# Kernel optimization log

Measured on AMD Instinct MI355X. Metric: run time of the kernel, lower is better.

## Reference

```python
import jax, jax.numpy as jnp
import numpy as np

B, T, S, D, H = 2, 2048, 2048, 2048, 16
HD = D // H  # 128
SCALE = 1.0 / np.sqrt(HD)


def _rope(x, cos, sin):
    # x: [B,H,S,HD]; cos/sin: [1,1,S,HD//2]
    b, h, s, d = x.shape
    xs = x.reshape(b, h, s, d // 2, 2)
    x0, x1 = xs[..., 0], xs[..., 1]
    rot = jnp.stack([x0 * cos - x1 * sin, x1 * cos + x0 * sin], axis=-1)
    return rot.reshape(b, h, s, d)


def _split_heads(x):
    b, s, _ = x.shape
    return x.reshape(b, s, H, HD).transpose(0, 2, 1, 3)


def setup_inputs() -> dict:
    key = jax.random.key(0)
    ks = jax.random.split(key, 6)
    w_std = (1.0 / np.sqrt(2.0)) * np.sqrt(6.0 / (D + D))  # xavier_uniform with gain 1/sqrt(2)
    def xavier(k):
        return jax.random.uniform(k, (D, D), jnp.float32, -w_std, w_std)
    # rotary tables (standard inv-freq form)
    inv_freq = 1.0 / (10000.0 ** (np.arange(0, HD, 2, dtype=np.float32) / HD))  # [HD//2]
    ang = np.arange(T, dtype=np.float32)[:, None] * inv_freq[None, :]           # [T,HD//2]
    cos = jnp.asarray(np.cos(ang), jnp.float32)[None, None]  # [1,1,T,HD//2]
    sin = jnp.asarray(np.sin(ang), jnp.float32)[None, None]
    return {
        "hidden_states": jax.random.normal(ks[0], (B, T, D), jnp.float32),
        "encoder_hidden_states": jax.random.normal(ks[1], (B, S, D), jnp.float32),
        "Wq": xavier(ks[2]),
        "Wk": xavier(ks[3]),
        "Wv": xavier(ks[4]),
        "Wo": xavier(ks[5]),
        "cos_q": cos, "sin_q": sin,
        "cos_k": cos, "sin_k": sin,
    }


def reference(hidden_states, encoder_hidden_states, Wq, Wk, Wv, Wo,
              cos_q, sin_q, cos_k, sin_k):
    # Linear (no bias): y = x @ W.T
    q = _split_heads(jnp.einsum('btd,ed->bte', hidden_states, Wq))          # [B,H,T,HD]
    k = _split_heads(jnp.einsum('bsd,ed->bse', encoder_hidden_states, Wk))  # [B,H,S,HD]
    v = _split_heads(jnp.einsum('bsd,ed->bse', encoder_hidden_states, Wv))  # [B,H,S,HD]
    q = _rope(q, cos_q, sin_q)
    k = _rope(k, cos_k, sin_k)
    scores = jnp.einsum('bhtd,bhsd->bhts', q, k) * SCALE                    # [B,H,T,S]
    attn = jax.nn.softmax(scores.astype(jnp.float32), axis=-1)
    ctx = jnp.einsum('bhts,bhsd->bhtd', attn, v)                            # [B,H,T,HD]
    ctx = ctx.transpose(0, 2, 1, 3).reshape(B, T, D)                        # merge heads
    return jnp.einsum('btd,ed->bte', ctx, Wo)
```

## Files before the change

kernel.cpp:

```cpp
#include <hip/hip_runtime.h>
#include <cmath>

#define SCALE_F 0.088388347648318447f

typedef _Float16 f16;
typedef _Float16 f16x8 __attribute__((ext_vector_type(8)));
typedef _Float16 f16x4 __attribute__((ext_vector_type(4)));
typedef float f32x4 __attribute__((ext_vector_type(4)));
typedef float f32x16 __attribute__((ext_vector_type(16)));
typedef unsigned int u32;
typedef unsigned int u32x4 __attribute__((ext_vector_type(4)));

#define MFMA16(a, b, c) __builtin_amdgcn_mfma_f32_16x16x32_f16(a, b, c, 0, 0, 0)
#define MFMA32(a, b, c) __builtin_amdgcn_mfma_f32_32x32x16_f16(a, b, c, 0, 0, 0)
#define Z16 ((f32x16){0.f,0.f,0.f,0.f,0.f,0.f,0.f,0.f,0.f,0.f,0.f,0.f,0.f,0.f,0.f,0.f})
#define EX2(x) __builtin_amdgcn_exp2f(x)

__device__ __forceinline__ void gl2lds16(const f16* g, f16* l) {
    __builtin_amdgcn_global_load_lds(
        (const __attribute__((address_space(1))) unsigned int*)g,
        (__attribute__((address_space(3))) unsigned int*)l, 16, 0, 0);
}

__device__ __forceinline__ u32 pk2(float x, float y) {
    const unsigned short a = __builtin_bit_cast(unsigned short, (f16)x);
    const unsigned short b = __builtin_bit_cast(unsigned short, (f16)y);
    return (u32)a | ((u32)b << 16);
}
__device__ __forceinline__ float fswapsum(float x) {
    u32 a = __builtin_bit_cast(u32, x), b;
    asm volatile("v_mov_b32 %0, %1" : "=&v"(b) : "v"(a));
    asm volatile("v_permlane32_swap_b32 %0, %1" : "+v"(a), "+v"(b));
    return __builtin_bit_cast(float, a) + __builtin_bit_cast(float, b);
}
__device__ __forceinline__ float fswapmax(float x) {
    u32 a = __builtin_bit_cast(u32, x), b;
    asm volatile("v_mov_b32 %0, %1" : "=&v"(b) : "v"(a));
    asm volatile("v_permlane32_swap_b32 %0, %1" : "+v"(a), "+v"(b));
    return fmaxf(__builtin_bit_cast(float, a), __builtin_bit_cast(float, b));
}

__global__ __launch_bounds__(256) void cvt_all(
    const float* __restrict__ hs, const float* __restrict__ es,
    const float* __restrict__ Wq, const float* __restrict__ Wk,
    const float* __restrict__ Wv, const float* __restrict__ Wo,
    f16* __restrict__ dst)
{
    const int c = blockIdx.x * 256 + threadIdx.x;
    const float* src; int off;
    if (c < 2097152) { src = (c < 1048576) ? hs : es; off = c & 1048575; }
    else {
        const int cc = c - 2097152;
        const int wsel = cc >> 19; off = cc & 524287;
        src = wsel == 0 ? Wq : wsel == 1 ? Wk : wsel == 2 ? Wv : Wo;
    }
    const float4* p = (const float4*)src + (size_t)off * 2;
    const float4 a = p[0], b2 = p[1];
    f16x8 o = {(f16)a.x, (f16)a.y, (f16)a.z, (f16)a.w,
               (f16)b2.x, (f16)b2.y, (f16)b2.z, (f16)b2.w};
    *(f16x8*)(dst + (size_t)c * 8) = o;
}

template <int OUT_MODE>
__global__ __launch_bounds__(256, 2) void gemm16(
    const f16* __restrict__ A, const f16* __restrict__ W,
    void* __restrict__ Cv, int M, int N, int K,
    const float* __restrict__ Cs, const float* __restrict__ Sn)
{
    __shared__ __align__(16) f16 Al[128 * 64];
    __shared__ __align__(16) f16 Bl[128 * 64];
    const int tid = threadIdx.x;
    const int l = tid & 63, w = tid >> 6;
    const int wr = w >> 1, wc = w & 1;

    const int nwg = gridDim.x, cpx = nwg >> 3;
    const int bid = blockIdx.x;
    const int swz = (bid & 7) * cpx + (bid >> 3);
    const int nbn = N >> 7;
    const int bm = (swz / nbn) * 128, bn = (swz % nbn) * 128;

    f32x4 acc[4][4];
#pragma unroll
    for (int i = 0; i < 4; ++i)
#pragma unroll
        for (int j = 0; j < 4; ++j) acc[i][j] = (f32x4){0.f, 0.f, 0.f, 0.f};

    const int srow = tid >> 3;
    const int sg = tid & 7;

    for (int k0 = 0; k0 < K; k0 += 64) {
        __syncthreads();
#pragma unroll
        for (int i = 0; i < 4; ++i) {
            const int row = i * 32 + srow;
            const int lg = sg ^ (row & 7);
            gl2lds16(A + (size_t)(bm + row) * K + k0 + lg * 8, Al + row * 64 + sg * 8);
            gl2lds16(W + (size_t)(bn + row) * K + k0 + lg * 8, Bl + row * 64 + sg * 8);
        }
        __syncthreads();
#pragma unroll
        for (int kk = 0; kk < 2; ++kk) {
            f16x8 a[4], b[4];
            const int g = kk * 4 + (l >> 4);
#pragma unroll
            for (int m = 0; m < 4; ++m) {
                const int row = wr * 64 + m * 16 + (l & 15);
                a[m] = *(const f16x8*)(Al + row * 64 + (g ^ (row & 7)) * 8);
            }
#pragma unroll
            for (int n = 0; n < 4; ++n) {
                const int row = wc * 64 + n * 16 + (l & 15);
                b[n] = *(const f16x8*)(Bl + row * 64 + (g ^ (row & 7)) * 8);
            }
#pragma unroll
            for (int m = 0; m < 4; ++m)
#pragma unroll
                for (int n = 0; n < 4; ++n)
                    acc[m][n] = MFMA16(a[m], b[n], acc[m][n]);
        }
    }

#pragma unroll
    for (int m = 0; m < 4; ++m)
#pragma unroll
        for (int n = 0; n < 4; ++n)
#pragma unroll
            for (int j = 0; j < 4; ++j) {
                const int r = bm + wr * 64 + m * 16 + ((l >> 4) << 2) + j;
                const int c = bn + wc * 64 + n * 16 + (l & 15);
                if (OUT_MODE == 0) {
                    ((f16*)Cv)[(size_t)r * N + c] = (f16)acc[m][n][j];
                } else if (OUT_MODE == 2) {
                    ((float*)Cv)[(size_t)r * N + c] = acc[m][n][j];
                } else if (OUT_MODE == 3) {
                    ((f16*)Cv)[(size_t)((c >> 11) * 2048 + r) * 2048 + (c & 2047)] = (f16)acc[m][n][j];
                } else if (OUT_MODE == 4) {
                    const float v = acc[m][n][j];
                    const float vp = __shfl_xor(v, 1);
                    const int t = r & 2047;
                    const int i2 = (c & 127) >> 1;
                    const float co = Cs[t * 64 + i2];
                    const float si = Sn[t * 64 + i2];
                    const float y = (c & 1) ? fmaf(v, co, vp * si) : fmaf(v, co, -vp * si);
                    ((f16*)Cv)[(size_t)r * N + c] = (f16)y;
                }
            }
}

__global__ __launch_bounds__(256, 2) void attn16(
    const f16* __restrict__ Qg, const f16* __restrict__ Kg,
    const f16* __restrict__ Vt, f16* __restrict__ Og)
{
    __shared__ __align__(16) f16 Kl[2][64 * 128];
    __shared__ __align__(16) f16 Vl[2][128 * 64];
    __shared__ float bnc[4][32];

    const int tid = threadIdx.x;
    const int l = tid & 63, w = tid >> 6;
    const int l31 = l & 31, hi = l >> 5;
    const int hi4 = hi * 4;

    const int bid = blockIdx.x;
    const int swz = (bid & 7) * 64 + (bid >> 3);
    const int bh = swz >> 4, qt = swz & 15;
    const int b = bh >> 4, h = bh & 15;

    const int qrow = b * 2048 + qt * 128 + w * 32 + l31;
    const f16 qsc = (f16)(0.088388347648318447f * 1.44269504088896f);
    f16x8 qf[8];
#pragma unroll
    for (int kc = 0; kc < 8; ++kc) {
        f16x8 t0 = *(const f16x8*)(Qg + (size_t)qrow * 2048 + h * 128 + kc * 16 + hi * 8);
#pragma unroll
        for (int e = 0; e < 8; ++e) t0[e] = t0[e] * qsc;
        qf[kc] = t0;
    }

    f32x16 o[4] = {Z16, Z16, Z16, Z16};
    float mrow = -3.0e38f, lrow = 0.0f;

    const f16* Kbase = Kg + (size_t)(b * 2048) * 2048 + h * 128;
    const f16* Vbase = Vt + (size_t)(b * 2048 + h * 128) * 2048;

#define STAGE(buf, st) do {                                                              \
    _Pragma("unroll")                                                                    \
    for (int u = 0; u < 4; ++u) {                                                        \
        const int idx = u * 256 + tid; const int row = idx >> 4, g = idx & 15;           \
        gl2lds16(Kbase + (size_t)((st) + row) * 2048 + (g ^ (row & 15)) * 8,             \
                 &Kl[buf][row * 128 + g * 8]);                                           \
    }                                                                                    \
    _Pragma("unroll")                                                                    \
    for (int u = 0; u < 4; ++u) {                                                        \
        const int idx = u * 256 + tid; const int d = idx >> 3, g = idx & 7;              \
        gl2lds16(Vbase + (size_t)d * 2048 + (st) + (g ^ (d & 7)) * 8,                    \
                 &Vl[buf][d * 64 + g * 8]);                                              \
    }                                                                                    \
} while (0)

    STAGE(0, 0);
    __syncthreads();

    int cur = 0;
    for (int t = 0; t < 32; ++t) {
        if (t < 31) STAGE(cur ^ 1, (t + 1) * 64);
        const f16* Kc = Kl[cur];
        const f16* Vc = Vl[cur];

        f32x16 p0 = Z16, p1 = Z16;
        __builtin_amdgcn_s_setprio(1);
#pragma unroll
        for (int kc = 0; kc < 8; ++kc) {
            const int g = ((kc * 2 + hi) ^ (l31 & 15)) * 8;
            const f16x8 k0 = *(const f16x8*)(Kc + l31 * 128 + g);
            const f16x8 k1 = *(const f16x8*)(Kc + (32 + l31) * 128 + g);
            p0 = MFMA32(k0, qf[kc], p0);
            p1 = MFMA32(k1, qf[kc], p1);
        }
        __builtin_amdgcn_s_setprio(0);

        float mt[16];
#pragma unroll
        for (int r = 0; r < 16; ++r) mt[r] = fmaxf(p0[r], p1[r]);
#pragma unroll
        for (int r = 0; r < 8; ++r) mt[r] = fmaxf(mt[r], mt[r + 8]);
#pragma unroll
        for (int r = 0; r < 4; ++r) mt[r] = fmaxf(mt[r], mt[r + 4]);
        float mx = fmaxf(fmaxf(mt[0], mt[1]), fmaxf(mt[2], mt[3]));
        mx = fswapmax(mx);

        if (!__all(mx <= mrow + 8.0f)) {
            const float mn = fmaxf(mrow, mx);
            const float cr = EX2(mrow - mn);
            mrow = mn;
            lrow *= cr;
            if (hi == 0) bnc[w][l31] = cr;
#pragma unroll
            for (int r = 0; r < 16; ++r) {
                const float crr = bnc[w][(r & 3) + 8 * (r >> 2) + 4 * hi];
                o[0][r] *= crr; o[1][r] *= crr; o[2][r] *= crr; o[3][r] *= crr;
            }
        }

        float st16[16];
#pragma unroll
        for (int r = 0; r < 16; ++r) {
            p0[r] = EX2(p0[r] - mrow);
            p1[r] = EX2(p1[r] - mrow);
            st16[r] = p0[r] + p1[r];
        }
#pragma unroll
        for (int r = 0; r < 8; ++r) st16[r] += st16[r + 8];
#pragma unroll
        for (int r = 0; r < 4; ++r) st16[r] += st16[r + 4];
        lrow += fswapsum((st16[0] + st16[1]) + (st16[2] + st16[3]));

        f16x8 pf[4];
#pragma unroll
        for (int ksl = 0; ksl < 2; ++ksl) {
            u32x4 w0 = {pk2(p0[8*ksl+0], p0[8*ksl+1]), pk2(p0[8*ksl+2], p0[8*ksl+3]),
                        pk2(p0[8*ksl+4], p0[8*ksl+5]), pk2(p0[8*ksl+6], p0[8*ksl+7])};
            pf[ksl] = __builtin_bit_cast(f16x8, w0);
            u32x4 w1 = {pk2(p1[8*ksl+0], p1[8*ksl+1]), pk2(p1[8*ksl+2], p1[8*ksl+3]),
                        pk2(p1[8*ksl+4], p1[8*ksl+5]), pk2(p1[8*ksl+6], p1[8*ksl+7])};
            pf[2 + ksl] = __builtin_bit_cast(f16x8, w1);
        }

        __builtin_amdgcn_s_setprio(1);
#pragma unroll
        for (int dt = 0; dt < 4; ++dt) {
            const f16* vrow = Vc + (dt * 32 + l31) * 64;
#pragma unroll
            for (int ks = 0; ks < 4; ++ks) {
                const f16x4 vlo = *(const f16x4*)(vrow + ((ks * 2)     ^ (l31 & 7)) * 8 + hi4);
                const f16x4 vhi = *(const f16x4*)(vrow + ((ks * 2 + 1) ^ (l31 & 7)) * 8 + hi4);
                const f16x8 vf = __builtin_shufflevector(vlo, vhi, 0, 1, 2, 3, 4, 5, 6, 7);
                o[dt] = MFMA32(pf[ks], vf, o[dt]);
            }
        }
        __builtin_amdgcn_s_setprio(0);

        __syncthreads();
        cur ^= 1;
    }
#undef STAGE

    const float inv = 1.0f / lrow;
    if (hi == 0) bnc[w][l31] = inv;
#pragma unroll
    for (int r = 0; r < 16; ++r) {
        const int qq = (r & 3) + 8 * (r >> 2) + 4 * hi;
        const float ir = bnc[w][qq];
        const size_t row = (size_t)(b * 2048 + qt * 128 + w * 32 + qq);
#pragma unroll
        for (int dt = 0; dt < 4; ++dt)
            Og[row * 2048 + h * 128 + dt * 32 + l31] = (f16)(o[dt][r] * ir);
    }
}

extern "C" void kernel_launch(void* const* d_in, const int* in_sizes, int n_in,
                              void* d_out, int out_size, void* d_ws, size_t ws_size,
                              hipStream_t stream) {
    const float* hs = (const float*)d_in[0];
    const float* es = (const float*)d_in[1];
    const float* Wq = (const float*)d_in[2];
    const float* Wk = (const float*)d_in[3];
    const float* Wv = (const float*)d_in[4];
    const float* Wo = (const float*)d_in[5];
    const float* cq = (const float*)d_in[6];
    const float* sq = (const float*)d_in[7];
    const float* ck = (const float*)d_in[8];
    const float* sk = (const float*)d_in[9];
    float* out = (float*)d_out;

    f16* hs16 = (f16*)d_ws;
    f16* es16 = hs16 + 8388608;
    f16* Wq16 = es16 + 8388608;
    f16* Wk16 = Wq16 + 4194304;
    f16* Wv16 = Wk16 + 4194304;
    f16* Wo16 = Wv16 + 4194304;
    f16* Q16  = Wo16 + 4194304;
    f16* K16  = Q16 + 8388608;
    f16* Vt16 = K16 + 8388608;
    f16* ctx16 = hs16;

    const dim3 tB(256);
    cvt_all<<<dim3(16384), tB, 0, stream>>>(hs, es, Wq, Wk, Wv, Wo, hs16);

    gemm16<4><<<dim3(512), tB, 0, stream>>>(hs16, Wq16, Q16, 4096, 2048, 2048, cq, sq);
    gemm16<4><<<dim3(512), tB, 0, stream>>>(es16, Wk16, K16, 4096, 2048, 2048, ck, sk);
    gemm16<3><<<dim3(512), tB, 0, stream>>>(Wv16, es16, Vt16, 2048, 4096, 2048, nullptr, nullptr);

    attn16<<<dim3(512), tB, 0, stream>>>(Q16, K16, Vt16, ctx16);

    gemm16<2><<<dim3(512), tB, 0, stream>>>(ctx16, Wo16, out, 4096, 2048, 2048, nullptr, nullptr);
}
```

Measured before the change: 292.6 us.

## Stage K/V through registers into padded LDS instead of direct global-to-LDS loads

New measurement: 290.1 us. Within noise of the previous version (-0.8%).

```diff
diff --git a/kernel.cpp b/kernel.cpp
--- a/kernel.cpp
+++ b/kernel.cpp
@@ -9,6 +9,7 @@
 typedef float f32x4 __attribute__((ext_vector_type(4)));
 typedef float f32x16 __attribute__((ext_vector_type(16)));
 typedef unsigned int u32;
+typedef unsigned int u32x2 __attribute__((ext_vector_type(2)));
 typedef unsigned int u32x4 __attribute__((ext_vector_type(4)));
 
 #define MFMA16(a, b, c) __builtin_amdgcn_mfma_f32_16x16x32_f16(a, b, c, 0, 0, 0)
@@ -151,8 +152,8 @@
     const f16* __restrict__ Qg, const f16* __restrict__ Kg,
     const f16* __restrict__ Vt, f16* __restrict__ Og)
 {
-    __shared__ __align__(16) f16 Kl[2][64 * 128];
-    __shared__ __align__(16) f16 Vl[2][128 * 64];
+    __shared__ __align__(16) f16 Kl[2][64 * 132];
+    __shared__ __align__(16) f16 Vl[2][128 * 68];
     __shared__ float bnc[4][32];
 
     const int tid = threadIdx.x;
@@ -160,6 +161,9 @@
     const int l31 = l & 31, hi = l >> 5;
     const int hi4 = hi * 4;
 
+    const int krow = tid >> 4, kg = tid & 15;
+    const int vd = tid >> 3, vg = tid & 7;
+
     const int bid = blockIdx.x;
     const int swz = (bid & 7) * 64 + (bid >> 3);
     const int bh = swz >> 4, qt = swz & 15;
@@ -182,27 +186,39 @@
     const f16* Kbase = Kg + (size_t)(b * 2048) * 2048 + h * 128;
     const f16* Vbase = Vt + (size_t)(b * 2048 + h * 128) * 2048;
 
-#define STAGE(buf, st) do {                                                              \
+    u32x4 kst[4], vst[4];
+
+#define LOADT(st) do {                                                                   \
+    _Pragma("unroll")                                                                    \
+    for (int u = 0; u < 4; ++u)                                                          \
+        kst[u] = *(const u32x4*)(Kbase + (size_t)((st) + krow + u * 16) * 2048 + kg * 8);\
+    _Pragma("unroll")                                                                    \
+    for (int u = 0; u < 4; ++u)                                                          \
+        vst[u] = *(const u32x4*)(Vbase + (size_t)(vd + u * 32) * 2048 + (st) + vg * 8);  \
+} while (0)
+
+#define WRITET(bf) do {                                                                  \
     _Pragma("unroll")                                                                    \
     for (int u = 0; u < 4; ++u) {                                                        \
-        const int idx = u * 256 + tid; const int row = idx >> 4, g = idx & 15;           \
-        gl2lds16(Kbase + (size_t)((st) + row) * 2048 + (g ^ (row & 15)) * 8,             \
-                 &Kl[buf][row * 128 + g * 8]);                                           \
+        f16* p = &Kl[bf][(krow + u * 16) * 132 + kg * 8];                                \
+        *(u32x2*)p       = (u32x2){kst[u].x, kst[u].y};                                  \
+        *(u32x2*)(p + 4) = (u32x2){kst[u].z, kst[u].w};                                  \
     }                                                                                    \
     _Pragma("unroll")                                                                    \
     for (int u = 0; u < 4; ++u) {                                                        \
-        const int idx = u * 256 + tid; const int d = idx >> 3, g = idx & 7;              \
-        gl2lds16(Vbase + (size_t)d * 2048 + (st) + (g ^ (d & 7)) * 8,                    \
-                 &Vl[buf][d * 64 + g * 8]);                                              \
+        f16* p = &Vl[bf][(vd + u * 32) * 68 + vg * 8];                                   \
+        *(u32x2*)p       = (u32x2){vst[u].x, vst[u].y};                                  \
+        *(u32x2*)(p + 4) = (u32x2){vst[u].z, vst[u].w};                                  \
     }                                                                                    \
 } while (0)
 
-    STAGE(0, 0);
+    LOADT(0);
+    WRITET(0);
     __syncthreads();
 
     int cur = 0;
     for (int t = 0; t < 32; ++t) {
-        if (t < 31) STAGE(cur ^ 1, (t + 1) * 64);
+        if (t < 31) LOADT((t + 1) * 64);
         const f16* Kc = Kl[cur];
         const f16* Vc = Vl[cur];
 
@@ -210,9 +226,13 @@
         __builtin_amdgcn_s_setprio(1);
 #pragma unroll
         for (int kc = 0; kc < 8; ++kc) {
-            const int g = ((kc * 2 + hi) ^ (l31 & 15)) * 8;
-            const f16x8 k0 = *(const f16x8*)(Kc + l31 * 128 + g);
-            const f16x8 k1 = *(const f16x8*)(Kc + (32 + l31) * 128 + g);
+            const int go = (kc * 2 + hi) * 8;
+            const f16* kp0 = Kc + l31 * 132 + go;
+            const f16* kp1 = Kc + (32 + l31) * 132 + go;
+            const f16x4 a0 = *(const f16x4*)kp0, a1 = *(const f16x4*)(kp0 + 4);
+            const f16x4 b0 = *(const f16x4*)kp1, b1 = *(const f16x4*)(kp1 + 4);
+            const f16x8 k0 = __builtin_shufflevector(a0, a1, 0, 1, 2, 3, 4, 5, 6, 7);
+            const f16x8 k1 = __builtin_shufflevector(b0, b1, 0, 1, 2, 3, 4, 5, 6, 7);
             p0 = MFMA32(k0, qf[kc], p0);
             p1 = MFMA32(k1, qf[kc], p1);
         }
@@ -265,14 +285,16 @@
             pf[2 + ksl] = __builtin_bit_cast(f16x8, w1);
         }
 
+        if (t < 31) WRITET(cur ^ 1);
+
         __builtin_amdgcn_s_setprio(1);
 #pragma unroll
         for (int dt = 0; dt < 4; ++dt) {
-            const f16* vrow = Vc + (dt * 32 + l31) * 64;
+            const f16* vrow = Vc + (dt * 32 + l31) * 68;
 #pragma unroll
             for (int ks = 0; ks < 4; ++ks) {
-                const f16x4 vlo = *(const f16x4*)(vrow + ((ks * 2)     ^ (l31 & 7)) * 8 + hi4);
-                const f16x4 vhi = *(const f16x4*)(vrow + ((ks * 2 + 1) ^ (l31 & 7)) * 8 + hi4);
+                const f16x4 vlo = *(const f16x4*)(vrow + ks * 16 + hi4);
+                const f16x4 vhi = *(const f16x4*)(vrow + ks * 16 + hi4 + 8);
                 const f16x8 vf = __builtin_shufflevector(vlo, vhi, 0, 1, 2, 3, 4, 5, 6, 7);
                 o[dt] = MFMA32(pf[ks], vf, o[dt]);
             }
@@ -282,7 +304,8 @@
         __syncthreads();
         cur ^= 1;
     }
-#undef STAGE
+#undef LOADT
+#undef WRITET
 
     const float inv = 1.0f / lrow;
     if (hi == 0) bnc[w][l31] = inv;
```
